# Kernel optimization log

Hardware: AMD Instinct MI355X
Metric: run time of the kernel (lower is better)

The kernel has to match this reference:

```python
import jax, jax.numpy as jnp
import numpy as np


def setup_inputs() -> dict:
    key = jax.random.key(0)
    ks = jax.random.split(key, 7)
    T, B, D, H, Q = 256, 128, 1024, 2048, 1024
    return {
        "x": jax.random.normal(ks[0], (T, B, D), dtype=jnp.float32),
        "h0": jax.random.normal(ks[1], (B, H), dtype=jnp.float32) * 0.01,
        "W_xh": jax.random.normal(ks[2], (D, H), dtype=jnp.float32) * 0.01,
        "W_hh": jax.random.normal(ks[3], (H, H), dtype=jnp.float32) * 0.01,
        "b_h": jnp.zeros((H,), dtype=jnp.float32),
        "W_hq": jax.random.normal(ks[4], (H, Q), dtype=jnp.float32) * 0.01,
        "b_q": jnp.zeros((Q,), dtype=jnp.float32),
    }


def reference(x, h0, W_xh, W_hh, b_h, W_hq, b_q):
    # x: (T, B, D); vanilla RNN recurrence with ReLU, per-step output projection.
    def step(h, xt):
        h = jax.nn.relu(xt @ W_xh + h @ W_hh + b_h)  # (B, H)
        return h, h @ W_hq + b_q                      # (B, Q)

    h, outs = jax.lax.scan(step, h0, x)               # outs: (T, B, Q)
    out = outs.reshape(-1, outs.shape[-1])            # torch.cat along dim 0 -> (T*B, Q)
    return out, h
```

## Files before the change

kernel.cpp:

```cpp
#include <hip/hip_runtime.h>
#include <hip/hip_bf16.h>

typedef __bf16 bf16_t;
typedef bf16_t bf16x8 __attribute__((ext_vector_type(8)));
typedef bf16_t bf16x4 __attribute__((ext_vector_type(4)));
typedef bf16_t bf16x2 __attribute__((ext_vector_type(2)));
typedef float f32x4 __attribute__((ext_vector_type(4)));
typedef float f32x2 __attribute__((ext_vector_type(2)));

__device__ __forceinline__ void load_lds16(const bf16_t* g, bf16_t* l) {
  __builtin_amdgcn_global_load_lds(
      (const __attribute__((address_space(1))) unsigned int*)g,
      (__attribute__((address_space(3))) unsigned int*)l,
      16, 0, 0);
}

__global__ void conv_f32_bf16(const float* __restrict__ src,
                              bf16_t* __restrict__ dst, long n) {
  long i = ((long)blockIdx.x * blockDim.x + threadIdx.x) * 8;
  if (i + 7 >= n) return;
  float4 a = *(const float4*)(src + i);
  float4 b = *(const float4*)(src + i + 4);
  bf16x8 v;
  v[0] = (bf16_t)a.x; v[1] = (bf16_t)a.y; v[2] = (bf16_t)a.z; v[3] = (bf16_t)a.w;
  v[4] = (bf16_t)b.x; v[5] = (bf16_t)b.y; v[6] = (bf16_t)b.z; v[7] = (bf16_t)b.w;
  *(bf16x8*)(dst + i) = v;
}

__global__ void conv_bf16_f32(const bf16_t* __restrict__ src,
                              float* __restrict__ dst, long n) {
  long i = (long)blockIdx.x * blockDim.x + threadIdx.x;
  if (i >= n) return;
  dst[i] = (float)src[i];
}

__global__ void transpose_conv(const float* __restrict__ src,
                               bf16_t* __restrict__ dst, int Ksrc, int Nsrc) {
  __shared__ float tile[32][33];
  int n0 = blockIdx.x * 32, k0 = blockIdx.y * 32;
  int tx = threadIdx.x, ty = threadIdx.y;
#pragma unroll
  for (int i = 0; i < 32; i += 8)
    tile[ty + i][tx] = src[(long)(k0 + ty + i) * Nsrc + n0 + tx];
  __syncthreads();
#pragma unroll
  for (int i = 0; i < 32; i += 8)
    dst[(long)(n0 + ty + i) * Ksrc + k0 + tx] = (bf16_t)tile[tx][ty + i];
}

template <int STORE_MODE>
__global__ __launch_bounds__(256) void gemm_bt_128(
    const bf16_t* __restrict__ A, const bf16_t* __restrict__ Bt,
    const float* __restrict__ bias, void* __restrict__ Dout,
    int M, int N, int K) {
  __shared__ bf16_t As[128 * 32];
  __shared__ bf16_t Bs[128 * 32];
  const int tid = threadIdx.x;
  const int lane = tid & 63;
  const int w = tid >> 6;
  const int wr = w >> 1, wc = w & 1;
  const int m0 = blockIdx.y * 128, n0 = blockIdx.x * 128;

  f32x4 acc[4][4] = {};

  const int r0 = tid >> 2;
  const int kk = (tid & 3) * 8;
  const int fr = lane & 15;
  const int fk = (lane >> 4) * 8;

  for (int k0 = 0; k0 < K; k0 += 32) {
    load_lds16(A + (long)(m0 + r0) * K + k0 + kk, As + w * 512);
    load_lds16(A + (long)(m0 + 64 + r0) * K + k0 + kk, As + 2048 + w * 512);
    load_lds16(Bt + (long)(n0 + r0) * K + k0 + kk, Bs + w * 512);
    load_lds16(Bt + (long)(n0 + 64 + r0) * K + k0 + kk, Bs + 2048 + w * 512);
    asm volatile("s_waitcnt vmcnt(0)" ::: "memory");
    __syncthreads();

    bf16x8 af[4], bfx[4];
#pragma unroll
    for (int m = 0; m < 4; ++m)
      af[m] = *(const bf16x8*)&As[(wr * 64 + m * 16 + fr) * 32 + fk];
#pragma unroll
    for (int n = 0; n < 4; ++n)
      bfx[n] = *(const bf16x8*)&Bs[(wc * 64 + n * 16 + fr) * 32 + fk];
#pragma unroll
    for (int m = 0; m < 4; ++m)
#pragma unroll
      for (int n = 0; n < 4; ++n)
        acc[m][n] = __builtin_amdgcn_mfma_f32_16x16x32_bf16(af[m], bfx[n],
                                                            acc[m][n], 0, 0, 0);
    __syncthreads();
  }

  const int fq = lane >> 4;
#pragma unroll
  for (int m = 0; m < 4; ++m) {
#pragma unroll
    for (int n = 0; n < 4; ++n) {
      int col = n0 + wc * 64 + n * 16 + fr;
      float bv = bias[col];
#pragma unroll
      for (int r = 0; r < 4; ++r) {
        int row = m0 + wr * 64 + m * 16 + fq * 4 + r;
        float v = acc[m][n][r] + bv;
        if (STORE_MODE == 0)
          ((float*)Dout)[(long)row * N + col] = v;
        else
          ((bf16_t*)Dout)[(long)row * N + col] = (bf16_t)v;
      }
    }
  }
}

__device__ __forceinline__ void half_bar(unsigned int* c, unsigned int target,
                                         int lane) {
  if (lane == 0)
    __hip_atomic_fetch_add(c, 1u, __ATOMIC_RELEASE,
                           __HIP_MEMORY_SCOPE_WORKGROUP);
  unsigned int v;
  do {
    v = __hip_atomic_load(c, __ATOMIC_ACQUIRE, __HIP_MEMORY_SCOPE_WORKGROUP);
    if (v >= target) break;
    __builtin_amdgcn_s_sleep(1);
  } while (true);
}

__global__ __launch_bounds__(512, 1) void rnn_persistent13(
    const bf16_t* __restrict__ h0,
    bf16_t* __restrict__ Hbuf,
    const bf16_t* __restrict__ WhhT,
    unsigned int* __restrict__ flags) {
  __shared__ bf16_t Wlds[65536];
  __shared__ float sred[2][4][16 * 36];
  __shared__ unsigned int barc[2];
  __shared__ unsigned int sfree[2];

  const int tid = threadIdx.x, lane = tid & 63, w = tid >> 6;
  const int h = w >> 2;
  const int lw = w & 3;
  const int gid = blockIdx.x;
  const int p = (gid >> 1) & 3;
  const int n0idx = ((gid & 1) << 5) | (gid >> 3);
  const int chain = p + h * 4;
  const int m0 = chain * 16, n0 = n0idx * 32;
  const int H = 2048;
  const long BH = 128L * 2048;
  const int kb = lw * 512;
  const int fr = lane & 15, fg = lane >> 4;
  const int w64 = lw * 64;

  {
    const int scol = tid >> 4;
    const int sk16 = tid & 15;
    const bf16_t* gsrc = WhhT + (long)(n0 + scol) * H + sk16 * 8;
#pragma unroll 4
    for (int j = 0; j < 16; ++j) {
      bf16x8 v = *(const bf16x8*)(gsrc + j * 128);
      int k8 = sk16 + j * 16;
      *(bf16x8*)&Wlds[(k8 * 32 + scol) * 8] = v;
    }
  }
  if (tid < 2) { barc[tid] = 0; sfree[tid] = 0; }
  __syncthreads();

  if (h == 1) __builtin_amdgcn_s_sleep(64);

  const int zrowW = lane >> 2, zcolW = (lane & 3) * 8;
  const int sidx = zrowW * 36 + zcolW;
  const long zoffW = (long)(m0 + zrowW) * H + n0 + zcolW;

  unsigned int* myflag = flags + (((chain << 6) | n0idx) << 4);
  const unsigned int* pollflag =
      flags + (((chain << 6) | (lw * 16 + (lane & 15))) << 4);
  unsigned int* bc = &barc[h];
  unsigned int* sf = &sfree[h];

  for (int t = 0; t < 256; ++t) {
    const bf16_t* hp = (t == 0) ? h0 : Hbuf + (long)(t - 1) * BH;
    bf16_t* z = Hbuf + (long)t * BH;
    const int ew = t & 3;

    f32x4 zvr;
    if (lw == ew) {
      const bf16_t* zp = z + zoffW;
      asm volatile("global_load_dwordx4 %0, %1, off sc0 sc1"
                   : "=v"(zvr)
                   : "v"(zp)
                   : "memory");
    }

    if (t > 0) {
      const unsigned int tt = (unsigned int)t;
      unsigned int v = __hip_atomic_load(pollflag, __ATOMIC_RELAXED,
                                         __HIP_MEMORY_SCOPE_AGENT);
      if (!__all(v >= tt)) {
        __builtin_amdgcn_s_sleep(1);
        v = __hip_atomic_load(pollflag, __ATOMIC_RELAXED,
                              __HIP_MEMORY_SCOPE_AGENT);
        if (!__all(v >= tt)) {
          __builtin_amdgcn_s_sleep(2);
          v = __hip_atomic_load(pollflag, __ATOMIC_RELAXED,
                                __HIP_MEMORY_SCOPE_AGENT);
          if (!__all(v >= tt)) {
            __builtin_amdgcn_s_sleep(4);
            v = __hip_atomic_load(pollflag, __ATOMIC_RELAXED,
                                  __HIP_MEMORY_SCOPE_AGENT);
            while (!__all(v >= tt)) {
              __builtin_amdgcn_s_sleep(8);
              v = __hip_atomic_load(pollflag, __ATOMIC_RELAXED,
                                    __HIP_MEMORY_SCOPE_AGENT);
            }
          }
        }
      }
    }

    const bf16_t* Ab = hp + (long)(m0 + fr) * H + kb + fg * 8;
    f32x4 a0, a1, a2, a3, a4, a5, a6, a7, a8, a9, a10, a11, a12, a13, a14, a15;
    asm volatile(
        "global_load_dwordx4 %0, %16, off sc0\n\t"
        "global_load_dwordx4 %1, %16, off offset:64 sc0\n\t"
        "global_load_dwordx4 %2, %16, off offset:128 sc0\n\t"
        "global_load_dwordx4 %3, %16, off offset:192 sc0\n\t"
        "global_load_dwordx4 %4, %16, off offset:256 sc0\n\t"
        "global_load_dwordx4 %5, %16, off offset:320 sc0\n\t"
        "global_load_dwordx4 %6, %16, off offset:384 sc0\n\t"
        "global_load_dwordx4 %7, %16, off offset:448 sc0\n\t"
        "global_load_dwordx4 %8, %16, off offset:512 sc0\n\t"
        "global_load_dwordx4 %9, %16, off offset:576 sc0\n\t"
        "global_load_dwordx4 %10, %16, off offset:640 sc0\n\t"
        "global_load_dwordx4 %11, %16, off offset:704 sc0\n\t"
        "global_load_dwordx4 %12, %16, off offset:768 sc0\n\t"
        "global_load_dwordx4 %13, %16, off offset:832 sc0\n\t"
        "global_load_dwordx4 %14, %16, off offset:896 sc0\n\t"
        "global_load_dwordx4 %15, %16, off offset:960 sc0"
        : "=&v"(a0), "=&v"(a1), "=&v"(a2), "=&v"(a3), "=&v"(a4), "=&v"(a5),
          "=&v"(a6), "=&v"(a7), "=&v"(a8), "=&v"(a9), "=&v"(a10), "=&v"(a11),
          "=&v"(a12), "=&v"(a13), "=&v"(a14), "=&v"(a15)
        : "v"(Ab)
        : "memory");

    f32x4 acc0 = {}, acc1 = {};
#define STEPX(ks, A)                                                          \
  {                                                                           \
    bf16x8 w0 = *(const bf16x8*)&Wlds[((w64 + (ks) * 4 + fg) * 32 + fr) * 8]; \
    bf16x8 w1 =                                                               \
        *(const bf16x8*)&Wlds[((w64 + (ks) * 4 + fg) * 32 + 16 + fr) * 8];    \
    bf16x8 av = __builtin_bit_cast(bf16x8, A);                                \
    acc0 = __builtin_amdgcn_mfma_f32_16x16x32_bf16(av, w0, acc0, 0, 0, 0);    \
    acc1 = __builtin_amdgcn_mfma_f32_16x16x32_bf16(av, w1, acc1, 0, 0, 0);    \
  }
    asm volatile("s_waitcnt vmcnt(8)" ::: "memory");
    __builtin_amdgcn_sched_barrier(0);
    STEPX(0, a0)   STEPX(1, a1)   STEPX(2, a2)   STEPX(3, a3)
    STEPX(4, a4)   STEPX(5, a5)   STEPX(6, a6)   STEPX(7, a7)
    asm volatile("s_waitcnt vmcnt(0)" ::: "memory");
    __builtin_amdgcn_sched_barrier(0);
    STEPX(8, a8)   STEPX(9, a9)   STEPX(10, a10) STEPX(11, a11)
    STEPX(12, a12) STEPX(13, a13) STEPX(14, a14) STEPX(15, a15)
#undef STEPX

    if (t > 0) {
      while (__hip_atomic_load(sf, __ATOMIC_ACQUIRE,
                               __HIP_MEMORY_SCOPE_WORKGROUP) <
             (unsigned int)t)
        __builtin_amdgcn_s_sleep(1);
    }

#pragma unroll
    for (int rr = 0; rr < 4; ++rr) {
      sred[h][lw][(fg * 4 + rr) * 36 + fr] = acc0[rr];
      sred[h][lw][(fg * 4 + rr) * 36 + 16 + fr] = acc1[rr];
    }
    half_bar(bc, (unsigned int)(t + 1) * 4, lane);

    if (lw == ew) {
      f32x4 slo = *(const f32x4*)&sred[h][0][sidx];
      f32x4 shi = *(const f32x4*)&sred[h][0][sidx + 4];
#pragma unroll
      for (int ww = 1; ww < 4; ++ww) {
        slo = slo + *(const f32x4*)&sred[h][ww][sidx];
        shi = shi + *(const f32x4*)&sred[h][ww][sidx + 4];
      }
      bf16x8 zv = __builtin_bit_cast(bf16x8, zvr);
      bf16x8 o;
#pragma unroll
      for (int c = 0; c < 4; ++c) {
        float v0 = slo[c] + (float)zv[c];
        float v1 = shi[c] + (float)zv[c + 4];
        o[c] = (bf16_t)(v0 > 0.f ? v0 : 0.f);
        o[c + 4] = (bf16_t)(v1 > 0.f ? v1 : 0.f);
      }
      const bf16_t* zp = z + zoffW;
      {
        f32x4 ov = __builtin_bit_cast(f32x4, o);
        asm volatile("global_store_dwordx4 %0, %1, off sc0 sc1" ::"v"(zp),
                     "v"(ov)
                     : "memory");
      }
      asm volatile("s_waitcnt vmcnt(0)" ::: "memory");
      if (lane == 0) {
        __hip_atomic_store(myflag, (unsigned int)(t + 1), __ATOMIC_RELAXED,
                           __HIP_MEMORY_SCOPE_AGENT);
        __hip_atomic_store(sf, (unsigned int)(t + 1), __ATOMIC_RELEASE,
                           __HIP_MEMORY_SCOPE_WORKGROUP);
      }
    }
  }
}

extern "C" void kernel_launch(void* const* d_in, const int* in_sizes, int n_in,
                              void* d_out, int out_size, void* d_ws,
                              size_t ws_size, hipStream_t stream) {
  const float* x   = (const float*)d_in[0];
  const float* h0  = (const float*)d_in[1];
  const float* Wxh = (const float*)d_in[2];
  const float* Whh = (const float*)d_in[3];
  const float* bh  = (const float*)d_in[4];
  const float* Whq = (const float*)d_in[5];
  const float* bq  = (const float*)d_in[6];
  float* out = (float*)d_out;

  const int T = 256, B = 128, D = 1024, H = 2048, Q = 1024;
  const long MB = (long)T * B;

  char* ws = (char*)d_ws;
  unsigned int* flags = (unsigned int*)ws;  ws += 512 * 64;
  bf16_t* x_bf = (bf16_t*)ws;  ws += MB * D * 2;
  bf16_t* Hbuf = (bf16_t*)ws;  ws += MB * H * 2;
  bf16_t* h0bf = (bf16_t*)ws;  ws += (long)B * H * 2;
  bf16_t* WxhT = (bf16_t*)ws;  ws += (long)H * D * 2;
  bf16_t* WhhT = (bf16_t*)ws;  ws += (long)H * H * 2;
  bf16_t* WhqT = (bf16_t*)ws;  ws += (long)Q * H * 2;

  hipMemsetAsync(flags, 0, 512 * 64, stream);

  conv_f32_bf16<<<(int)(MB * D / 8 / 256), 256, 0, stream>>>(x, x_bf, MB * D);
  conv_f32_bf16<<<(int)((long)B * H / 8 / 256), 256, 0, stream>>>(h0, h0bf,
                                                                  (long)B * H);
  transpose_conv<<<dim3(H / 32, D / 32), dim3(32, 8), 0, stream>>>(Wxh, WxhT, D, H);
  transpose_conv<<<dim3(H / 32, H / 32), dim3(32, 8), 0, stream>>>(Whh, WhhT, H, H);
  transpose_conv<<<dim3(Q / 32, H / 32), dim3(32, 8), 0, stream>>>(Whq, WhqT, H, Q);

  gemm_bt_128<1><<<dim3(H / 128, MB / 128), 256, 0, stream>>>(
      x_bf, WxhT, bh, Hbuf, (int)MB, H, D);

  rnn_persistent13<<<256, 512, 0, stream>>>(h0bf, Hbuf, WhhT, flags);

  gemm_bt_128<0><<<dim3(Q / 128, MB / 128), 256, 0, stream>>>(
      Hbuf, WhqT, bq, out, (int)MB, Q, H);

  conv_bf16_f32<<<(int)((long)B * H / 256), 256, 0, stream>>>(
      Hbuf + (long)(T - 1) * B * H, out + MB * Q, (long)B * H);
}
```

Measured before the change: 1.731 ms.

## Fuse output projection into persistent RNN kernel using register-pinned Whq slices

```diff
diff --git a/kernel.cpp b/kernel.cpp
--- a/kernel.cpp
+++ b/kernel.cpp
@@ -125,15 +125,21 @@
   } while (true);
 }
 
-__global__ __launch_bounds__(512, 1) void rnn_persistent13(
+__global__ __launch_bounds__(512, 1) void rnn_persistent14(
     const bf16_t* __restrict__ h0,
     bf16_t* __restrict__ Hbuf,
     const bf16_t* __restrict__ WhhT,
+    const bf16_t* __restrict__ WhqT,
+    const float* __restrict__ bq,
+    float* __restrict__ out,
     unsigned int* __restrict__ flags) {
   __shared__ bf16_t Wlds[65536];
   __shared__ float sred[2][4][16 * 36];
+  __shared__ bf16_t qred[2][4][16 * 20];
   __shared__ unsigned int barc[2];
   __shared__ unsigned int sfree[2];
+  __shared__ unsigned int qbc[2];
+  __shared__ unsigned int qfree[2];
 
   const int tid = threadIdx.x, lane = tid & 63, w = tid >> 6;
   const int h = w >> 2;
@@ -148,6 +154,7 @@
   const int kb = lw * 512;
   const int fr = lane & 15, fg = lane >> 4;
   const int w64 = lw * 64;
+  const int qcol0 = n0idx * 16;
 
   {
     const int scol = tid >> 4;
@@ -160,7 +167,21 @@
       *(bf16x8*)&Wlds[(k8 * 32 + scol) * 8] = v;
     }
   }
-  if (tid < 2) { barc[tid] = 0; sfree[tid] = 0; }
+  if (tid < 2) { barc[tid] = 0; sfree[tid] = 0; qbc[tid] = 0; qfree[tid] = 0; }
+
+  const bf16_t* Wq = WhqT + (long)(qcol0 + fr) * H + kb + fg * 8;
+#define LOADPIN(dst, off)                                                     \
+  bf16x8 dst = *(const bf16x8*)(Wq + (off));                                  \
+  {                                                                           \
+    f32x4 t_ = __builtin_bit_cast(f32x4, dst);                                \
+    asm volatile("" : "+v"(t_));                                              \
+    dst = __builtin_bit_cast(bf16x8, t_);                                     \
+  }
+  LOADPIN(q0, 0)    LOADPIN(q1, 32)   LOADPIN(q2, 64)   LOADPIN(q3, 96)
+  LOADPIN(q4, 128)  LOADPIN(q5, 160)  LOADPIN(q6, 192)  LOADPIN(q7, 224)
+  LOADPIN(q8, 256)  LOADPIN(q9, 288)  LOADPIN(q10, 320) LOADPIN(q11, 352)
+  LOADPIN(q12, 384) LOADPIN(q13, 416) LOADPIN(q14, 448) LOADPIN(q15, 480)
+#undef LOADPIN
   __syncthreads();
 
   if (h == 1) __builtin_amdgcn_s_sleep(64);
@@ -168,17 +189,23 @@
   const int zrowW = lane >> 2, zcolW = (lane & 3) * 8;
   const int sidx = zrowW * 36 + zcolW;
   const long zoffW = (long)(m0 + zrowW) * H + n0 + zcolW;
+
+  const int qrow = lane >> 2, qc4 = (lane & 3) * 4;
+  const f32x4 bqv = *(const f32x4*)(bq + qcol0 + qc4);
 
   unsigned int* myflag = flags + (((chain << 6) | n0idx) << 4);
   const unsigned int* pollflag =
       flags + (((chain << 6) | (lw * 16 + (lane & 15))) << 4);
   unsigned int* bc = &barc[h];
   unsigned int* sf = &sfree[h];
+  unsigned int* qc = &qbc[h];
+  unsigned int* qf = &qfree[h];
 
   for (int t = 0; t < 256; ++t) {
     const bf16_t* hp = (t == 0) ? h0 : Hbuf + (long)(t - 1) * BH;
     bf16_t* z = Hbuf + (long)t * BH;
     const int ew = t & 3;
+    const int ew2 = (t + 2) & 3;
 
     f32x4 zvr;
     if (lw == ew) {
@@ -306,6 +333,107 @@
                            __HIP_MEMORY_SCOPE_WORKGROUP);
       }
     }
+
+    if (t > 0) {
+      f32x4 qacc = {};
+#define QSTEP(A, QW)                                                          \
+  qacc = __builtin_amdgcn_mfma_f32_16x16x32_bf16(                             \
+      __builtin_bit_cast(bf16x8, A), QW, qacc, 0, 0, 0);
+      QSTEP(a0, q0)   QSTEP(a1, q1)   QSTEP(a2, q2)   QSTEP(a3, q3)
+      QSTEP(a4, q4)   QSTEP(a5, q5)   QSTEP(a6, q6)   QSTEP(a7, q7)
+      QSTEP(a8, q8)   QSTEP(a9, q9)   QSTEP(a10, q10) QSTEP(a11, q11)
+      QSTEP(a12, q12) QSTEP(a13, q13) QSTEP(a14, q14) QSTEP(a15, q15)
+#undef QSTEP
+      while (__hip_atomic_load(qf, __ATOMIC_ACQUIRE,
+                               __HIP_MEMORY_SCOPE_WORKGROUP) <
+             (unsigned int)(t - 1))
+        __builtin_amdgcn_s_sleep(1);
+#pragma unroll
+      for (int rr = 0; rr < 4; ++rr)
+        qred[h][lw][(fg * 4 + rr) * 20 + fr] = (bf16_t)qacc[rr];
+      half_bar(qc, (unsigned int)t * 4, lane);
+
+      if (lw == ew2) {
+        f32x4 s = bqv;
+#pragma unroll
+        for (int ww = 0; ww < 4; ++ww)
+#pragma unroll
+          for (int j = 0; j < 4; ++j)
+            s[j] += (float)qred[h][ww][qrow * 20 + qc4 + j];
+        float* op = out + ((long)(t - 1) * 128 + m0 + qrow) * 1024 + qcol0 + qc4;
+        *(f32x4*)op = s;
+        if (lane == 0)
+          __hip_atomic_store(qf, (unsigned int)t, __ATOMIC_RELEASE,
+                             __HIP_MEMORY_SCOPE_WORKGROUP);
+      }
+    }
+  }
+
+  {
+    const unsigned int tt = 256u;
+    unsigned int v;
+    do {
+      v = __hip_atomic_load(pollflag, __ATOMIC_RELAXED,
+                            __HIP_MEMORY_SCOPE_AGENT);
+      if (__all(v >= tt)) break;
+      __builtin_amdgcn_s_sleep(2);
+    } while (true);
+
+    const bf16_t* hp = Hbuf + 255L * BH;
+    const bf16_t* Ab = hp + (long)(m0 + fr) * H + kb + fg * 8;
+    f32x4 a0, a1, a2, a3, a4, a5, a6, a7, a8, a9, a10, a11, a12, a13, a14, a15;
+    asm volatile(
+        "global_load_dwordx4 %0, %16, off sc0\n\t"
+        "global_load_dwordx4 %1, %16, off offset:64 sc0\n\t"
+        "global_load_dwordx4 %2, %16, off offset:128 sc0\n\t"
+        "global_load_dwordx4 %3, %16, off offset:192 sc0\n\t"
+        "global_load_dwordx4 %4, %16, off offset:256 sc0\n\t"
+        "global_load_dwordx4 %5, %16, off offset:320 sc0\n\t"
+        "global_load_dwordx4 %6, %16, off offset:384 sc0\n\t"
+        "global_load_dwordx4 %7, %16, off offset:448 sc0\n\t"
+        "global_load_dwordx4 %8, %16, off offset:512 sc0\n\t"
+        "global_load_dwordx4 %9, %16, off offset:576 sc0\n\t"
+        "global_load_dwordx4 %10, %16, off offset:640 sc0\n\t"
+        "global_load_dwordx4 %11, %16, off offset:704 sc0\n\t"
+        "global_load_dwordx4 %12, %16, off offset:768 sc0\n\t"
+        "global_load_dwordx4 %13, %16, off offset:832 sc0\n\t"
+        "global_load_dwordx4 %14, %16, off offset:896 sc0\n\t"
+        "global_load_dwordx4 %15, %16, off offset:960 sc0\n\t"
+        "s_waitcnt vmcnt(0)"
+        : "=&v"(a0), "=&v"(a1), "=&v"(a2), "=&v"(a3), "=&v"(a4), "=&v"(a5),
+          "=&v"(a6), "=&v"(a7), "=&v"(a8), "=&v"(a9), "=&v"(a10), "=&v"(a11),
+          "=&v"(a12), "=&v"(a13), "=&v"(a14), "=&v"(a15)
+        : "v"(Ab)
+        : "memory");
+    __builtin_amdgcn_sched_barrier(0);
+
+    f32x4 qacc = {};
+#define QSTEP(A, QW)                                                          \
+  qacc = __builtin_amdgcn_mfma_f32_16x16x32_bf16(                             \
+      __builtin_bit_cast(bf16x8, A), QW, qacc, 0, 0, 0);
+    QSTEP(a0, q0)   QSTEP(a1, q1)   QSTEP(a2, q2)   QSTEP(a3, q3)
+    QSTEP(a4, q4)   QSTEP(a5, q5)   QSTEP(a6, q6)   QSTEP(a7, q7)
+    QSTEP(a8, q8)   QSTEP(a9, q9)   QSTEP(a10, q10) QSTEP(a11, q11)
+    QSTEP(a12, q12) QSTEP(a13, q13) QSTEP(a14, q14) QSTEP(a15, q15)
+#undef QSTEP
+    while (__hip_atomic_load(qf, __ATOMIC_ACQUIRE,
+                             __HIP_MEMORY_SCOPE_WORKGROUP) < 255u)
+      __builtin_amdgcn_s_sleep(1);
+#pragma unroll
+    for (int rr = 0; rr < 4; ++rr)
+      qred[h][lw][(fg * 4 + rr) * 20 + fr] = (bf16_t)qacc[rr];
+    half_bar(qc, 256u * 4, lane);
+
+    if (lw == ((256 + 2) & 3)) {
+      f32x4 s = bqv;
+#pragma unroll
+      for (int ww = 0; ww < 4; ++ww)
+#pragma unroll
+        for (int j = 0; j < 4; ++j)
+          s[j] += (float)qred[h][ww][qrow * 20 + qc4 + j];
+      float* op = out + (255L * 128 + m0 + qrow) * 1024 + qcol0 + qc4;
+      *(f32x4*)op = s;
+    }
   }
 }
 
@@ -345,10 +473,8 @@
   gemm_bt_128<1><<<dim3(H / 128, MB / 128), 256, 0, stream>>>(
       x_bf, WxhT, bh, Hbuf, (int)MB, H, D);
 
-  rnn_persistent13<<<256, 512, 0, stream>>>(h0bf, Hbuf, WhhT, flags);
-
-  gemm_bt_128<0><<<dim3(Q / 128, MB / 128), 256, 0, stream>>>(
-      Hbuf, WhqT, bq, out, (int)MB, Q, H);
+  rnn_persistent14<<<256, 512, 0, stream>>>(h0bf, Hbuf, WhhT, WhqT, bq, out,
+                                            flags);
 
   conv_bf16_f32<<<(int)((long)B * H / 256), 256, 0, stream>>>(
       Hbuf + (long)(T - 1) * B * H, out + MB * Q, (long)B * H);
```

Result: faster. 1.564 ms (-9.7%).
